# Performance work log

Measured on AMD Instinct MI355X. Metric: run time of the kernel, lower is better.

Reference implementation:

```python
import jax, jax.numpy as jnp
import numpy as np

B, S, E, H, D = 2, 2048, 1024, 16, 64  # batch, seq(=max_seq_len), embed_dim, heads, atten_dim


def setup_inputs() -> dict:
    key = jax.random.key(0)
    ks = jax.random.split(key, 9)
    s = 0.02
    return {
        "x": jax.random.normal(ks[0], (B, S, E), jnp.float32),
        "Wq": jax.random.normal(ks[1], (H, E, D), jnp.float32) * s,
        "Wk": jax.random.normal(ks[2], (H, E, D), jnp.float32) * s,
        "Wv": jax.random.normal(ks[3], (H, E, D), jnp.float32) * s,
        "bq": jax.random.normal(ks[4], (H, D), jnp.float32) * s,
        "bk": jax.random.normal(ks[5], (H, D), jnp.float32) * s,
        "bv": jax.random.normal(ks[6], (H, D), jnp.float32) * s,
        "Wp": jax.random.normal(ks[7], (H * D, E), jnp.float32) * s,
        "bp": jax.random.normal(ks[8], (E,), jnp.float32) * s,
    }


def reference(x, Wq, Wk, Wv, bq, bk, bv, Wp, bp):
    scale = jnp.sqrt(jnp.float32(D))
    # per-head projections, all heads at once: [B,H,S,D]
    q = jnp.einsum("bse,hed->bhsd", x, Wq) + bq[:, None, :]
    k = jnp.einsum("bse,hed->bhsd", x, Wk) + bk[:, None, :]
    v = jnp.einsum("bse,hed->bhsd", x, Wv) + bv[:, None, :]
    # causal scores [B,H,S,S], additive -inf mask above diagonal (as in the buffer)
    score = jnp.einsum("bhsd,bhtd->bhst", q, k) / scale
    mask = jnp.triu(jnp.full((S, S), -jnp.inf, jnp.float32), k=1)
    score = score + mask
    probs = jax.nn.softmax(score, axis=-1)
    attn = jnp.einsum("bhst,bhtd->bhsd", probs, v)
    # concat heads -> [B,S,H*D], then projection + ReLU
    concat = attn.transpose(0, 2, 1, 3).reshape(B, S, H * D)
    out = jax.nn.relu(concat @ Wp + bp)
    return out
```

## Files before the change

kernel.cpp:

```cpp
#include <hip/hip_runtime.h>

#define S_LEN 2048
#define E_DIM 1024
#define H_NUM 16
#define D_DIM 64

typedef unsigned short u16;
using bf16x8 = __attribute__((ext_vector_type(8))) short;
using f32x4  = __attribute__((ext_vector_type(4))) float;

#define MFMA16(A, B, C) __builtin_amdgcn_mfma_f32_16x16x32_bf16(A, B, C, 0, 0, 0)

__device__ __forceinline__ u16 f2bf(float f) {
    unsigned u = __float_as_uint(f);
    u += 0x7fffu + ((u >> 16) & 1u);
    return (u16)(u >> 16);
}
__device__ __forceinline__ f32x4 fzero4() { f32x4 z; z[0]=0.f; z[1]=0.f; z[2]=0.f; z[3]=0.f; return z; }

__device__ __forceinline__ void gll16(const u16* g, u16* l) {
    __builtin_amdgcn_global_load_lds(
        (const __attribute__((address_space(1))) void*)g,
        (__attribute__((address_space(3))) void*)l, 16, 0, 0);
}

__global__ __launch_bounds__(256) void cvt_bf16(const float* __restrict__ in, u16* __restrict__ outp, int n) {
    int i4 = (blockIdx.x * 256 + threadIdx.x) * 4;
    if (i4 < n) {
        float4 f = *(const float4*)(in + i4);
        unsigned lo = (unsigned)f2bf(f.x) | ((unsigned)f2bf(f.y) << 16);
        unsigned hi = (unsigned)f2bf(f.z) | ((unsigned)f2bf(f.w) << 16);
        uint2 p; p.x = lo; p.y = hi;
        *(uint2*)(outp + i4) = p;
    }
}

__device__ __forceinline__ void cvt_t_tile(const float* __restrict__ bin, u16* __restrict__ bout,
                                           int R, int C, int r0, int c0) {
    __shared__ float t[64][65];
    const int tid = threadIdx.x;
    const int lr = tid >> 2, lc = (tid & 3) * 16;

    const float* src = bin + (size_t)(r0 + lr) * C + c0 + lc;
    #pragma unroll
    for (int j = 0; j < 4; j++) {
        float4 f = *(const float4*)(src + j * 4);
        t[lr][lc + j * 4 + 0] = f.x; t[lr][lc + j * 4 + 1] = f.y;
        t[lr][lc + j * 4 + 2] = f.z; t[lr][lc + j * 4 + 3] = f.w;
    }
    __syncthreads();

    u16* dst = bout + (size_t)(c0 + lr) * R + r0 + lc;
    u16 vals[16];
    #pragma unroll
    for (int i = 0; i < 16; i++) vals[i] = f2bf(t[lc + i][lr]);
    uint4 pa, pb;
    pa.x = vals[0] | (vals[1] << 16);  pa.y = vals[2] | (vals[3] << 16);
    pa.z = vals[4] | (vals[5] << 16);  pa.w = vals[6] | (vals[7] << 16);
    pb.x = vals[8] | (vals[9] << 16);  pb.y = vals[10] | (vals[11] << 16);
    pb.z = vals[12] | (vals[13] << 16); pb.w = vals[14] | (vals[15] << 16);
    *(uint4*)dst = pa;
    *(uint4*)(dst + 8) = pb;
}

__global__ __launch_bounds__(256) void cvt_bf16_t(const float* __restrict__ in, u16* __restrict__ outp,
                                                  int R, int C) {
    const float* bin = in + (size_t)blockIdx.z * R * C;
    u16* bout = outp + (size_t)blockIdx.z * R * C;
    cvt_t_tile(bin, bout, R, C, blockIdx.y * 64, blockIdx.x * 64);
}

__global__ __launch_bounds__(256) void cvt_w3_t(
    const float* __restrict__ Wq, const float* __restrict__ Wk, const float* __restrict__ Wv,
    u16* __restrict__ wqt, u16* __restrict__ wkt, u16* __restrict__ wvt) {
    const int which = blockIdx.z >> 4, bh = blockIdx.z & 15;
    const float* in = (which == 0) ? Wq : (which == 1) ? Wk : Wv;
    u16* outp = (which == 0) ? wqt : (which == 1) ? wkt : wvt;
    const float* bin = in + (size_t)bh * E_DIM * D_DIM;
    u16* bout = outp + (size_t)bh * E_DIM * D_DIM;
    cvt_t_tile(bin, bout, E_DIM, D_DIM, blockIdx.y * 64, 0);
}

__global__ __launch_bounds__(256) void qkv_gemm(
    const u16* __restrict__ xb, const u16* __restrict__ wcat,
    const float* __restrict__ bq, const float* __restrict__ bk, const float* __restrict__ bv,
    u16* __restrict__ oq, u16* __restrict__ okk, u16* __restrict__ ov)
{
    const int m0 = blockIdx.x * 128;
    const int n0 = blockIdx.y * 128;

    __shared__ u16 As[128 * 32];
    __shared__ u16 Bs[128 * 32];

    const int tid  = threadIdx.x;
    const int wave = tid >> 6, lane = tid & 63, quad = lane >> 4, l16 = lane & 15;
    const int mh = wave >> 1, nh = wave & 1;

    const int lrow = lane >> 2, lcol = (lane & 3) * 8;
    const u16* aBase = xb   + (size_t)(m0 + wave * 32 + lrow) * E_DIM + lcol;
    const u16* bBase = wcat + (size_t)(n0 + wave * 32 + lrow) * E_DIM + lcol;
    u16* aLds0 = &As[(wave * 32     ) * 32];
    u16* aLds1 = &As[(wave * 32 + 16) * 32];
    u16* bLds0 = &Bs[(wave * 32     ) * 32];
    u16* bLds1 = &Bs[(wave * 32 + 16) * 32];

    f32x4 acc[4][4];
    #pragma unroll
    for (int j = 0; j < 4; j++)
        #pragma unroll
        for (int mi = 0; mi < 4; mi++) acc[j][mi] = fzero4();

    for (int k0 = 0; k0 < E_DIM; k0 += 32) {
        __syncthreads();
        gll16(aBase + k0,                 aLds0);
        gll16(aBase + k0 + 16 * E_DIM,    aLds1);
        gll16(bBase + k0,                 bLds0);
        gll16(bBase + k0 + 16 * E_DIM,    bLds1);
        __syncthreads();

        bf16x8 af[4];
        #pragma unroll
        for (int mi = 0; mi < 4; mi++)
            af[mi] = *(const bf16x8*)(&As[(mh * 64 + mi * 16 + l16) * 32 + quad * 8]);
        #pragma unroll
        for (int j = 0; j < 4; j++) {
            bf16x8 bfv = *(const bf16x8*)(&Bs[(nh * 64 + j * 16 + l16) * 32 + quad * 8]);
            #pragma unroll
            for (int mi = 0; mi < 4; mi++)
                acc[j][mi] = MFMA16(af[mi], bfv, acc[j][mi]);
        }
    }

    u16* outp[3] = { oq, okk, ov };
    const float* biasp[3] = { bq, bk, bv };
    #pragma unroll
    for (int j = 0; j < 4; j++) {
        const int n = n0 + nh * 64 + j * 16 + l16;
        const int t = n >> 10, h = (n >> 6) & 15, d = n & 63;
        float bia = biasp[t][h * D_DIM + d];
        u16* dst = outp[t];
        #pragma unroll
        for (int mi = 0; mi < 4; mi++) {
            #pragma unroll
            for (int r = 0; r < 4; r++) {
                int m = m0 + mh * 64 + mi * 16 + quad * 4 + r;
                int b = m >> 11, s = m & 2047;
                dst[((size_t)(b * H_NUM + h) * S_LEN + s) * D_DIM + d] =
                    f2bf(acc[j][mi][r] + bia);
            }
        }
    }
}

__global__ __launch_bounds__(256) void attn_fwd(
    const u16* __restrict__ q, const u16* __restrict__ k, const u16* __restrict__ v,
    u16* __restrict__ concat)
{
    const int p  = blockIdx.x;
    const int qa = p, qb = 31 - p;
    const int h  = blockIdx.y;
    const int bb = blockIdx.z;

    const size_t headoff = (size_t)(bb * H_NUM + h) * S_LEN * D_DIM;
    const u16* qh = q + headoff;
    const u16* kh = k + headoff;
    const u16* vh = v + headoff;

    __shared__ u16 Qa[64 * 72];
    __shared__ u16 Qb[64 * 72];
    __shared__ u16 Ks[64 * 72];
    __shared__ u16 Vt[64 * 72];
    __shared__ u16 Ps[4][16 * 72];

    const int tid  = threadIdx.x;
    const int wave = tid >> 6, lane = tid & 63, quad = lane >> 4, l16 = lane & 15;

    const int srow = tid >> 2, scg = tid & 3;
    const int vsk  = lane, vdb = wave * 16;

    {
        const u16* qsa = qh + (size_t)(qa * 64 + srow) * D_DIM + scg * 16;
        const u16* qsb = qh + (size_t)(qb * 64 + srow) * D_DIM + scg * 16;
        *(uint4*)(&Qa[srow * 72 + scg * 16    ]) = *(const uint4*)(qsa);
        *(uint4*)(&Qa[srow * 72 + scg * 16 + 8]) = *(const uint4*)(qsa + 8);
        *(uint4*)(&Qb[srow * 72 + scg * 16    ]) = *(const uint4*)(qsb);
        *(uint4*)(&Qb[srow * 72 + scg * 16 + 8]) = *(const uint4*)(qsb + 8);
    }
    __syncthreads();

    bf16x8 aqa0 = *(const bf16x8*)(&Qa[(wave * 16 + l16) * 72 + quad * 8]);
    bf16x8 aqa1 = *(const bf16x8*)(&Qa[(wave * 16 + l16) * 72 + 32 + quad * 8]);
    bf16x8 aqb0 = *(const bf16x8*)(&Qb[(wave * 16 + l16) * 72 + quad * 8]);
    bf16x8 aqb1 = *(const bf16x8*)(&Qb[(wave * 16 + l16) * 72 + 32 + quad * 8]);

    f32x4 oa[4], ob[4];
    #pragma unroll
    for (int nt = 0; nt < 4; nt++) { oa[nt] = fzero4(); ob[nt] = fzero4(); }
    float la[4] = {0.f,0.f,0.f,0.f}, lb[4] = {0.f,0.f,0.f,0.f};

    uint4 kA, kB, vA, vB;
    {
        const u16* ksrc = kh + (size_t)srow * D_DIM + scg * 16;
        kA = *(const uint4*)(ksrc); kB = *(const uint4*)(ksrc + 8);
        const u16* vsrc = vh + (size_t)vsk * D_DIM + vdb;
        vA = *(const uint4*)(vsrc); vB = *(const uint4*)(vsrc + 8);
    }

    for (int kt = 0; kt <= qb; kt++) {
        __syncthreads();
        *(uint4*)(&Ks[srow * 72 + scg * 16    ]) = kA;
        *(uint4*)(&Ks[srow * 72 + scg * 16 + 8]) = kB;
        {
            unsigned w[8] = { vA.x, vA.y, vA.z, vA.w, vB.x, vB.y, vB.z, vB.w };
            #pragma unroll
            for (int j = 0; j < 8; j++) {
                Vt[(vdb + 2 * j    ) * 72 + vsk] = (u16)(w[j] & 0xffffu);
                Vt[(vdb + 2 * j + 1) * 72 + vsk] = (u16)(w[j] >> 16);
            }
        }
        __syncthreads();

        if (kt < qb) {
            const u16* ksrc = kh + (size_t)((kt + 1) * 64 + srow) * D_DIM + scg * 16;
            kA = *(const uint4*)(ksrc); kB = *(const uint4*)(ksrc + 8);
            const u16* vsrc = vh + (size_t)((kt + 1) * 64 + vsk) * D_DIM + vdb;
            vA = *(const uint4*)(vsrc); vB = *(const uint4*)(vsrc + 8);
        }

        const bool both = (kt <= qa);

        f32x4 sb[4], sa[4];
        #pragma unroll
        for (int nt = 0; nt < 4; nt++) {
            bf16x8 bk0 = *(const bf16x8*)(&Ks[(nt * 16 + l16) * 72 + quad * 8]);
            bf16x8 bk1 = *(const bf16x8*)(&Ks[(nt * 16 + l16) * 72 + 32 + quad * 8]);
            sb[nt] = fzero4();
            sb[nt] = MFMA16(aqb0, bk0, sb[nt]);
            sb[nt] = MFMA16(aqb1, bk1, sb[nt]);
            if (both) {
                sa[nt] = fzero4();
                sa[nt] = MFMA16(aqa0, bk0, sa[nt]);
                sa[nt] = MFMA16(aqa1, bk1, sa[nt]);
            }
        }

        bf16x8 apb0, apb1, apa0, apa1;
        {
            const int qrow0 = qb * 64 + wave * 16 + quad * 4;
            u16 pbv[4][4];
            #pragma unroll
            for (int nt = 0; nt < 4; nt++)
                #pragma unroll
                for (int r = 0; r < 4; r++) {
                    float sv = sb[nt][r] * 0.125f;
                    if (kt == qb) {
                        int kcol = kt * 64 + nt * 16 + l16;
                        if (kcol > qrow0 + r) sv = -3.0e38f;
                    }
                    float pe = __expf(sv);
                    lb[r] += pe;
                    pbv[nt][r] = f2bf(pe);
                }
            u16* pw = &Ps[wave][0];
            #pragma unroll
            for (int nt = 0; nt < 4; nt++)
                #pragma unroll
                for (int r = 0; r < 4; r++)
                    pw[(quad * 4 + r) * 72 + nt * 16 + l16] = pbv[nt][r];
            apb0 = *(const bf16x8*)(&Ps[wave][l16 * 72 + quad * 8]);
            apb1 = *(const bf16x8*)(&Ps[wave][l16 * 72 + 32 + quad * 8]);
        }
        if (both) {
            const int qrow0 = qa * 64 + wave * 16 + quad * 4;
            u16 pav[4][4];
            #pragma unroll
            for (int nt = 0; nt < 4; nt++)
                #pragma unroll
                for (int r = 0; r < 4; r++) {
                    float sv = sa[nt][r] * 0.125f;
                    if (kt == qa) {
                        int kcol = kt * 64 + nt * 16 + l16;
                        if (kcol > qrow0 + r) sv = -3.0e38f;
                    }
                    float pe = __expf(sv);
                    la[r] += pe;
                    pav[nt][r] = f2bf(pe);
                }
            u16* pw = &Ps[wave][0];
            #pragma unroll
            for (int nt = 0; nt < 4; nt++)
                #pragma unroll
                for (int r = 0; r < 4; r++)
                    pw[(quad * 4 + r) * 72 + nt * 16 + l16] = pav[nt][r];
            apa0 = *(const bf16x8*)(&Ps[wave][l16 * 72 + quad * 8]);
            apa1 = *(const bf16x8*)(&Ps[wave][l16 * 72 + 32 + quad * 8]);
        }

        #pragma unroll
        for (int nt = 0; nt < 4; nt++) {
            bf16x8 bv0 = *(const bf16x8*)(&Vt[(nt * 16 + l16) * 72 + quad * 8]);
            bf16x8 bv1 = *(const bf16x8*)(&Vt[(nt * 16 + l16) * 72 + 32 + quad * 8]);
            ob[nt] = MFMA16(apb0, bv0, ob[nt]);
            ob[nt] = MFMA16(apb1, bv1, ob[nt]);
            if (both) {
                oa[nt] = MFMA16(apa0, bv0, oa[nt]);
                oa[nt] = MFMA16(apa1, bv1, oa[nt]);
            }
        }
    }

    #pragma unroll
    for (int r = 0; r < 4; r++) {
        #pragma unroll
        for (int off = 1; off < 16; off <<= 1) {
            la[r] += __shfl_xor(la[r], off);
            lb[r] += __shfl_xor(lb[r], off);
        }
    }
    #pragma unroll
    for (int nt = 0; nt < 4; nt++) {
        #pragma unroll
        for (int r = 0; r < 4; r++) {
            int sqa = qa * 64 + wave * 16 + quad * 4 + r;
            int sqb = qb * 64 + wave * 16 + quad * 4 + r;
            concat[((size_t)(bb * S_LEN + sqa)) * E_DIM + h * D_DIM + nt * 16 + l16] =
                f2bf(oa[nt][r] / la[r]);
            concat[((size_t)(bb * S_LEN + sqb)) * E_DIM + h * D_DIM + nt * 16 + l16] =
                f2bf(ob[nt][r] / lb[r]);
        }
    }
}

__global__ __launch_bounds__(256) void out_proj(
    const u16* __restrict__ concat, const u16* __restrict__ wpt,
    const float* __restrict__ bp, float* __restrict__ out)
{
    const int m0 = blockIdx.x * 128;
    const int n0 = blockIdx.y * 128;

    __shared__ u16 As[128 * 40];
    __shared__ u16 Bs[128 * 40];

    const int tid  = threadIdx.x;
    const int wave = tid >> 6, lane = tid & 63, quad = lane >> 4, l16 = lane & 15;
    const int mh = wave >> 1, nh = wave & 1;

    const int arow = tid >> 1, acol = (tid & 1) * 16;

    const u16* aptr = concat + (size_t)(m0 + arow) * E_DIM + acol;
    const u16* bptr = wpt + (size_t)(n0 + arow) * E_DIM + acol;

    f32x4 acc[4][4];
    #pragma unroll
    for (int j = 0; j < 4; j++)
        #pragma unroll
        for (int mi = 0; mi < 4; mi++) acc[j][mi] = fzero4();

    uint4 pA0, pA1, pB0, pB1;
    pA0 = *(const uint4*)(aptr);     pA1 = *(const uint4*)(aptr + 8);
    pB0 = *(const uint4*)(bptr);     pB1 = *(const uint4*)(bptr + 8);

    for (int k0 = 0; k0 < E_DIM; k0 += 32) {
        __syncthreads();
        *(uint4*)(&As[arow * 40 + acol    ]) = pA0;
        *(uint4*)(&As[arow * 40 + acol + 8]) = pA1;
        *(uint4*)(&Bs[arow * 40 + acol    ]) = pB0;
        *(uint4*)(&Bs[arow * 40 + acol + 8]) = pB1;
        __syncthreads();

        if (k0 + 32 < E_DIM) {
            pA0 = *(const uint4*)(aptr + k0 + 32);  pA1 = *(const uint4*)(aptr + k0 + 40);
            pB0 = *(const uint4*)(bptr + k0 + 32);  pB1 = *(const uint4*)(bptr + k0 + 40);
        }

        bf16x8 af[4];
        #pragma unroll
        for (int mi = 0; mi < 4; mi++)
            af[mi] = *(const bf16x8*)(&As[(mh * 64 + mi * 16 + l16) * 40 + quad * 8]);
        #pragma unroll
        for (int j = 0; j < 4; j++) {
            bf16x8 bfv = *(const bf16x8*)(&Bs[(nh * 64 + j * 16 + l16) * 40 + quad * 8]);
            #pragma unroll
            for (int mi = 0; mi < 4; mi++)
                acc[j][mi] = MFMA16(af[mi], bfv, acc[j][mi]);
        }
    }

    #pragma unroll
    for (int j = 0; j < 4; j++) {
        int n = n0 + nh * 64 + j * 16 + l16;
        float bia = bp[n];
        #pragma unroll
        for (int mi = 0; mi < 4; mi++) {
            #pragma unroll
            for (int r = 0; r < 4; r++) {
                int m = m0 + mh * 64 + mi * 16 + quad * 4 + r;
                out[(size_t)m * E_DIM + n] = fmaxf(acc[j][mi][r] + bia, 0.f);
            }
        }
    }
}

extern "C" void kernel_launch(void* const* d_in, const int* in_sizes, int n_in,
                              void* d_out, int out_size, void* d_ws, size_t ws_size,
                              hipStream_t stream)
{
    (void)in_sizes; (void)n_in; (void)out_size; (void)ws_size;
    const float* x  = (const float*)d_in[0];
    const float* Wq = (const float*)d_in[1];
    const float* Wk = (const float*)d_in[2];
    const float* Wv = (const float*)d_in[3];
    const float* bq = (const float*)d_in[4];
    const float* bk = (const float*)d_in[5];
    const float* bv = (const float*)d_in[6];
    const float* Wp = (const float*)d_in[7];
    const float* bp = (const float*)d_in[8];
    float* out = (float*)d_out;

    const size_t QKV_ELEMS = (size_t)2 * H_NUM * S_LEN * D_DIM;
    const size_t W_ELEMS   = (size_t)H_NUM * E_DIM * D_DIM;

    u16* q   = (u16*)d_ws;
    u16* k   = q   + QKV_ELEMS;
    u16* v   = k   + QKV_ELEMS;
    u16* cc  = v   + QKV_ELEMS;
    u16* xb  = cc  + QKV_ELEMS;
    u16* wqt = xb  + QKV_ELEMS;
    u16* wkt = wqt + W_ELEMS;
    u16* wvt = wkt + W_ELEMS;
    u16* wpt = wvt + W_ELEMS;

    cvt_bf16<<<dim3(4096), 256, 0, stream>>>(x, xb, (int)QKV_ELEMS);
    cvt_w3_t<<<dim3(1, 16, 48), 256, 0, stream>>>(Wq, Wk, Wv, wqt, wkt, wvt);
    cvt_bf16_t<<<dim3(16, 16, 1), 256, 0, stream>>>(Wp, wpt, H_NUM * D_DIM, E_DIM);

    qkv_gemm<<<dim3(32, 24), 256, 0, stream>>>(xb, wqt, bq, bk, bv, q, k, v);
    attn_fwd<<<dim3(16, 16, 2), 256, 0, stream>>>(q, k, v, cc);
    out_proj<<<dim3(32, 8), 256, 0, stream>>>(cc, wpt, bp, out);
}
```

Before: 203.0 us.

## Pre-transpose V, fold softmax scale into Q, compute transposed scores

A new kernel transposes V once into a [bh, D, S] buffer (reusing the xb workspace), so the attention loop can store V tiles to shared memory with vector writes instead of per-element scattered transposed stores. The 1/sqrt(D) scale moves into the QKV GEMM epilogue for Q. The score MFMA now swaps operands to compute K·Q^T, which lets P be packed into 64-bit shared stores and the row-sum reduce to a scalar per lane with fewer shuffles. The cost is an extra kernel launch and an extra pass over V in global memory.

```diff
diff --git a/kernel.cpp b/kernel.cpp
--- a/kernel.cpp
+++ b/kernel.cpp
@@ -81,6 +81,30 @@
     cvt_t_tile(bin, bout, E_DIM, D_DIM, blockIdx.y * 64, 0);
 }
 
+__global__ __launch_bounds__(256) void vt_prep(const u16* __restrict__ v, u16* __restrict__ vt) {
+    const int st = blockIdx.x;
+    const int bhi = blockIdx.y;
+    __shared__ u16 t[64 * 72];
+    const int tid = threadIdx.x;
+    const int wave = tid >> 6, lane = tid & 63;
+
+    const u16* src = v + (size_t)bhi * S_LEN * D_DIM + (size_t)(st * 64 + lane) * D_DIM + wave * 16;
+    uint4 a = *(const uint4*)(src);
+    uint4 b = *(const uint4*)(src + 8);
+    unsigned w[8] = { a.x, a.y, a.z, a.w, b.x, b.y, b.z, b.w };
+    #pragma unroll
+    for (int j = 0; j < 8; j++) {
+        t[(wave * 16 + 2 * j    ) * 72 + lane] = (u16)(w[j] & 0xffffu);
+        t[(wave * 16 + 2 * j + 1) * 72 + lane] = (u16)(w[j] >> 16);
+    }
+    __syncthreads();
+
+    const int dr = tid >> 2, sc = (tid & 3) * 16;
+    u16* dst = vt + (size_t)bhi * D_DIM * S_LEN + (size_t)dr * S_LEN + st * 64 + sc;
+    *(uint4*)(dst    ) = *(const uint4*)(&t[dr * 72 + sc    ]);
+    *(uint4*)(dst + 8) = *(const uint4*)(&t[dr * 72 + sc + 8]);
+}
+
 __global__ __launch_bounds__(256) void qkv_gemm(
     const u16* __restrict__ xb, const u16* __restrict__ wcat,
     const float* __restrict__ bq, const float* __restrict__ bk, const float* __restrict__ bv,
@@ -138,6 +162,7 @@
         const int n = n0 + nh * 64 + j * 16 + l16;
         const int t = n >> 10, h = (n >> 6) & 15, d = n & 63;
         float bia = biasp[t][h * D_DIM + d];
+        const float scl = (t == 0) ? 0.125f : 1.0f;
         u16* dst = outp[t];
         #pragma unroll
         for (int mi = 0; mi < 4; mi++) {
@@ -146,14 +171,14 @@
                 int m = m0 + mh * 64 + mi * 16 + quad * 4 + r;
                 int b = m >> 11, s = m & 2047;
                 dst[((size_t)(b * H_NUM + h) * S_LEN + s) * D_DIM + d] =
-                    f2bf(acc[j][mi][r] + bia);
+                    f2bf((acc[j][mi][r] + bia) * scl);
             }
         }
     }
 }
 
 __global__ __launch_bounds__(256) void attn_fwd(
-    const u16* __restrict__ q, const u16* __restrict__ k, const u16* __restrict__ v,
+    const u16* __restrict__ q, const u16* __restrict__ k, const u16* __restrict__ vt,
     u16* __restrict__ concat)
 {
     const int p  = blockIdx.x;
@@ -162,21 +187,20 @@
     const int bb = blockIdx.z;
 
     const size_t headoff = (size_t)(bb * H_NUM + h) * S_LEN * D_DIM;
-    const u16* qh = q + headoff;
-    const u16* kh = k + headoff;
-    const u16* vh = v + headoff;
+    const u16* qh  = q  + headoff;
+    const u16* kh  = k  + headoff;
+    const u16* vth = vt + headoff;
 
     __shared__ u16 Qa[64 * 72];
     __shared__ u16 Qb[64 * 72];
     __shared__ u16 Ks[64 * 72];
-    __shared__ u16 Vt[64 * 72];
+    __shared__ u16 Vts[64 * 72];
     __shared__ u16 Ps[4][16 * 72];
 
     const int tid  = threadIdx.x;
     const int wave = tid >> 6, lane = tid & 63, quad = lane >> 4, l16 = lane & 15;
 
     const int srow = tid >> 2, scg = tid & 3;
-    const int vsk  = lane, vdb = wave * 16;
 
     {
         const u16* qsa = qh + (size_t)(qa * 64 + srow) * D_DIM + scg * 16;
@@ -188,145 +212,140 @@
     }
     __syncthreads();
 
-    bf16x8 aqa0 = *(const bf16x8*)(&Qa[(wave * 16 + l16) * 72 + quad * 8]);
-    bf16x8 aqa1 = *(const bf16x8*)(&Qa[(wave * 16 + l16) * 72 + 32 + quad * 8]);
-    bf16x8 aqb0 = *(const bf16x8*)(&Qb[(wave * 16 + l16) * 72 + quad * 8]);
-    bf16x8 aqb1 = *(const bf16x8*)(&Qb[(wave * 16 + l16) * 72 + 32 + quad * 8]);
+    bf16x8 bqa0 = *(const bf16x8*)(&Qa[(wave * 16 + l16) * 72 + quad * 8]);
+    bf16x8 bqa1 = *(const bf16x8*)(&Qa[(wave * 16 + l16) * 72 + 32 + quad * 8]);
+    bf16x8 bqb0 = *(const bf16x8*)(&Qb[(wave * 16 + l16) * 72 + quad * 8]);
+    bf16x8 bqb1 = *(const bf16x8*)(&Qb[(wave * 16 + l16) * 72 + 32 + quad * 8]);
 
     f32x4 oa[4], ob[4];
     #pragma unroll
     for (int nt = 0; nt < 4; nt++) { oa[nt] = fzero4(); ob[nt] = fzero4(); }
-    float la[4] = {0.f,0.f,0.f,0.f}, lb[4] = {0.f,0.f,0.f,0.f};
+    float la = 0.f, lb = 0.f;
 
     uint4 kA, kB, vA, vB;
     {
         const u16* ksrc = kh + (size_t)srow * D_DIM + scg * 16;
         kA = *(const uint4*)(ksrc); kB = *(const uint4*)(ksrc + 8);
-        const u16* vsrc = vh + (size_t)vsk * D_DIM + vdb;
+        const u16* vsrc = vth + (size_t)srow * S_LEN + scg * 16;
         vA = *(const uint4*)(vsrc); vB = *(const uint4*)(vsrc + 8);
     }
+
+    const int qga = qa * 64 + wave * 16 + l16;
+    const int qgb = qb * 64 + wave * 16 + l16;
 
     for (int kt = 0; kt <= qb; kt++) {
         __syncthreads();
         *(uint4*)(&Ks[srow * 72 + scg * 16    ]) = kA;
         *(uint4*)(&Ks[srow * 72 + scg * 16 + 8]) = kB;
-        {
-            unsigned w[8] = { vA.x, vA.y, vA.z, vA.w, vB.x, vB.y, vB.z, vB.w };
-            #pragma unroll
-            for (int j = 0; j < 8; j++) {
-                Vt[(vdb + 2 * j    ) * 72 + vsk] = (u16)(w[j] & 0xffffu);
-                Vt[(vdb + 2 * j + 1) * 72 + vsk] = (u16)(w[j] >> 16);
-            }
-        }
+        *(uint4*)(&Vts[srow * 72 + scg * 16    ]) = vA;
+        *(uint4*)(&Vts[srow * 72 + scg * 16 + 8]) = vB;
         __syncthreads();
 
         if (kt < qb) {
             const u16* ksrc = kh + (size_t)((kt + 1) * 64 + srow) * D_DIM + scg * 16;
             kA = *(const uint4*)(ksrc); kB = *(const uint4*)(ksrc + 8);
-            const u16* vsrc = vh + (size_t)((kt + 1) * 64 + vsk) * D_DIM + vdb;
+            const u16* vsrc = vth + (size_t)srow * S_LEN + (kt + 1) * 64 + scg * 16;
             vA = *(const uint4*)(vsrc); vB = *(const uint4*)(vsrc + 8);
         }
 
         const bool both = (kt <= qa);
 
-        f32x4 sb[4], sa[4];
+        f32x4 stb[4], sta[4];
         #pragma unroll
         for (int nt = 0; nt < 4; nt++) {
-            bf16x8 bk0 = *(const bf16x8*)(&Ks[(nt * 16 + l16) * 72 + quad * 8]);
-            bf16x8 bk1 = *(const bf16x8*)(&Ks[(nt * 16 + l16) * 72 + 32 + quad * 8]);
-            sb[nt] = fzero4();
-            sb[nt] = MFMA16(aqb0, bk0, sb[nt]);
-            sb[nt] = MFMA16(aqb1, bk1, sb[nt]);
+            bf16x8 ak0 = *(const bf16x8*)(&Ks[(nt * 16 + l16) * 72 + quad * 8]);
+            bf16x8 ak1 = *(const bf16x8*)(&Ks[(nt * 16 + l16) * 72 + 32 + quad * 8]);
+            stb[nt] = fzero4();
+            stb[nt] = MFMA16(ak0, bqb0, stb[nt]);
+            stb[nt] = MFMA16(ak1, bqb1, stb[nt]);
             if (both) {
-                sa[nt] = fzero4();
-                sa[nt] = MFMA16(aqa0, bk0, sa[nt]);
-                sa[nt] = MFMA16(aqa1, bk1, sa[nt]);
-            }
-        }
-
-        bf16x8 apb0, apb1, apa0, apa1;
+                sta[nt] = fzero4();
+                sta[nt] = MFMA16(ak0, bqa0, sta[nt]);
+                sta[nt] = MFMA16(ak1, bqa1, sta[nt]);
+            }
+        }
+
         {
-            const int qrow0 = qb * 64 + wave * 16 + quad * 4;
-            u16 pbv[4][4];
-            #pragma unroll
-            for (int nt = 0; nt < 4; nt++)
-                #pragma unroll
-                for (int r = 0; r < 4; r++) {
-                    float sv = sb[nt][r] * 0.125f;
-                    if (kt == qb) {
-                        int kcol = kt * 64 + nt * 16 + l16;
-                        if (kcol > qrow0 + r) sv = -3.0e38f;
+            u16* pw = &Ps[wave][0];
+            #pragma unroll
+            for (int nt = 0; nt < 4; nt++) {
+                float pe[4];
+                if (kt == qb) {
+                    #pragma unroll
+                    for (int r = 0; r < 4; r++) {
+                        int kkg = kt * 64 + nt * 16 + quad * 4 + r;
+                        pe[r] = (kkg > qgb) ? 0.f : __expf(stb[nt][r]);
                     }
-                    float pe = __expf(sv);
-                    lb[r] += pe;
-                    pbv[nt][r] = f2bf(pe);
+                } else {
+                    #pragma unroll
+                    for (int r = 0; r < 4; r++) pe[r] = __expf(stb[nt][r]);
                 }
+                lb += pe[0] + pe[1] + pe[2] + pe[3];
+                uint2 pk;
+                pk.x = (unsigned)f2bf(pe[0]) | ((unsigned)f2bf(pe[1]) << 16);
+                pk.y = (unsigned)f2bf(pe[2]) | ((unsigned)f2bf(pe[3]) << 16);
+                *(uint2*)(&pw[l16 * 72 + nt * 16 + quad * 4]) = pk;
+            }
+            bf16x8 ap0 = *(const bf16x8*)(&Ps[wave][l16 * 72 + quad * 8]);
+            bf16x8 ap1 = *(const bf16x8*)(&Ps[wave][l16 * 72 + 32 + quad * 8]);
+            #pragma unroll
+            for (int nt = 0; nt < 4; nt++) {
+                bf16x8 bv0 = *(const bf16x8*)(&Vts[(nt * 16 + l16) * 72 + quad * 8]);
+                bf16x8 bv1 = *(const bf16x8*)(&Vts[(nt * 16 + l16) * 72 + 32 + quad * 8]);
+                ob[nt] = MFMA16(ap0, bv0, ob[nt]);
+                ob[nt] = MFMA16(ap1, bv1, ob[nt]);
+            }
+        }
+
+        if (both) {
             u16* pw = &Ps[wave][0];
             #pragma unroll
-            for (int nt = 0; nt < 4; nt++)
-                #pragma unroll
-                for (int r = 0; r < 4; r++)
-                    pw[(quad * 4 + r) * 72 + nt * 16 + l16] = pbv[nt][r];
-            apb0 = *(const bf16x8*)(&Ps[wave][l16 * 72 + quad * 8]);
-            apb1 = *(const bf16x8*)(&Ps[wave][l16 * 72 + 32 + quad * 8]);
-        }
-        if (both) {
-            const int qrow0 = qa * 64 + wave * 16 + quad * 4;
-            u16 pav[4][4];
-            #pragma unroll
-            for (int nt = 0; nt < 4; nt++)
-                #pragma unroll
-                for (int r = 0; r < 4; r++) {
-                    float sv = sa[nt][r] * 0.125f;
-                    if (kt == qa) {
-                        int kcol = kt * 64 + nt * 16 + l16;
-                        if (kcol > qrow0 + r) sv = -3.0e38f;
+            for (int nt = 0; nt < 4; nt++) {
+                float pe[4];
+                if (kt == qa) {
+                    #pragma unroll
+                    for (int r = 0; r < 4; r++) {
+                        int kkg = kt * 64 + nt * 16 + quad * 4 + r;
+                        pe[r] = (kkg > qga) ? 0.f : __expf(sta[nt][r]);
                     }
-                    float pe = __expf(sv);
-                    la[r] += pe;
-                    pav[nt][r] = f2bf(pe);
+                } else {
+                    #pragma unroll
+                    for (int r = 0; r < 4; r++) pe[r] = __expf(sta[nt][r]);
                 }
-            u16* pw = &Ps[wave][0];
-            #pragma unroll
-            for (int nt = 0; nt < 4; nt++)
-                #pragma unroll
-                for (int r = 0; r < 4; r++)
-                    pw[(quad * 4 + r) * 72 + nt * 16 + l16] = pav[nt][r];
-            apa0 = *(const bf16x8*)(&Ps[wave][l16 * 72 + quad * 8]);
-            apa1 = *(const bf16x8*)(&Ps[wave][l16 * 72 + 32 + quad * 8]);
-        }
-
+                la += pe[0] + pe[1] + pe[2] + pe[3];
+                uint2 pk;
+                pk.x = (unsigned)f2bf(pe[0]) | ((unsigned)f2bf(pe[1]) << 16);
+                pk.y = (unsigned)f2bf(pe[2]) | ((unsigned)f2bf(pe[3]) << 16);
+                *(uint2*)(&pw[l16 * 72 + nt * 16 + quad * 4]) = pk;
+            }
+            bf16x8 ap0 = *(const bf16x8*)(&Ps[wave][l16 * 72 + quad * 8]);
+            bf16x8 ap1 = *(const bf16x8*)(&Ps[wave][l16 * 72 + 32 + quad * 8]);
+            #pragma unroll
+            for (int nt = 0; nt < 4; nt++) {
+                bf16x8 bv0 = *(const bf16x8*)(&Vts[(nt * 16 + l16) * 72 + quad * 8]);
+                bf16x8 bv1 = *(const bf16x8*)(&Vts[(nt * 16 + l16) * 72 + 32 + quad * 8]);
+                oa[nt] = MFMA16(ap0, bv0, oa[nt]);
+                oa[nt] = MFMA16(ap1, bv1, oa[nt]);
+            }
+        }
+    }
+
+    lb += __shfl_xor(lb, 16); lb += __shfl_xor(lb, 32);
+    la += __shfl_xor(la, 16); la += __shfl_xor(la, 32);
+
+    #pragma unroll
+    for (int r = 0; r < 4; r++) {
+        const int srcl = quad * 4 + r;
+        float lbr = __shfl(lb, srcl);
+        float lar = __shfl(la, srcl);
+        int sqa = qa * 64 + wave * 16 + quad * 4 + r;
+        int sqb = qb * 64 + wave * 16 + quad * 4 + r;
         #pragma unroll
         for (int nt = 0; nt < 4; nt++) {
-            bf16x8 bv0 = *(const bf16x8*)(&Vt[(nt * 16 + l16) * 72 + quad * 8]);
-            bf16x8 bv1 = *(const bf16x8*)(&Vt[(nt * 16 + l16) * 72 + 32 + quad * 8]);
-            ob[nt] = MFMA16(apb0, bv0, ob[nt]);
-            ob[nt] = MFMA16(apb1, bv1, ob[nt]);
-            if (both) {
-                oa[nt] = MFMA16(apa0, bv0, oa[nt]);
-                oa[nt] = MFMA16(apa1, bv1, oa[nt]);
-            }
-        }
-    }
-
-    #pragma unroll
-    for (int r = 0; r < 4; r++) {
-        #pragma unroll
-        for (int off = 1; off < 16; off <<= 1) {
-            la[r] += __shfl_xor(la[r], off);
-            lb[r] += __shfl_xor(lb[r], off);
-        }
-    }
-    #pragma unroll
-    for (int nt = 0; nt < 4; nt++) {
-        #pragma unroll
-        for (int r = 0; r < 4; r++) {
-            int sqa = qa * 64 + wave * 16 + quad * 4 + r;
-            int sqb = qb * 64 + wave * 16 + quad * 4 + r;
             concat[((size_t)(bb * S_LEN + sqa)) * E_DIM + h * D_DIM + nt * 16 + l16] =
-                f2bf(oa[nt][r] / la[r]);
+                f2bf(oa[nt][r] / lar);
             concat[((size_t)(bb * S_LEN + sqb)) * E_DIM + h * D_DIM + nt * 16 + l16] =
-                f2bf(ob[nt][r] / lb[r]);
+                f2bf(ob[nt][r] / lbr);
         }
     }
 }
@@ -429,12 +448,14 @@
     u16* wkt = wqt + W_ELEMS;
     u16* wvt = wkt + W_ELEMS;
     u16* wpt = wvt + W_ELEMS;
+    u16* vtr = xb;
 
     cvt_bf16<<<dim3(4096), 256, 0, stream>>>(x, xb, (int)QKV_ELEMS);
     cvt_w3_t<<<dim3(1, 16, 48), 256, 0, stream>>>(Wq, Wk, Wv, wqt, wkt, wvt);
     cvt_bf16_t<<<dim3(16, 16, 1), 256, 0, stream>>>(Wp, wpt, H_NUM * D_DIM, E_DIM);
 
     qkv_gemm<<<dim3(32, 24), 256, 0, stream>>>(xb, wqt, bq, bk, bv, q, k, v);
-    attn_fwd<<<dim3(16, 16, 2), 256, 0, stream>>>(q, k, v, cc);
+    vt_prep<<<dim3(32, 32), 256, 0, stream>>>(v, vtr);
+    attn_fwd<<<dim3(16, 16, 2), 256, 0, stream>>>(q, k, vtr, cc);
     out_proj<<<dim3(32, 8), 256, 0, stream>>>(cc, wpt, bp, out);
 }
```

New measurement: 200.4 us. About the same (-1.3%).
